# Optimization experiments

Measured on AMD Instinct MI355X. Metric: run time of the kernel, lower is better.

## Reference

```python
import jax, jax.numpy as jnp
import numpy as np

MATCH_TIMES = 4  # init kwarg match_times


def box_xyxy_to_cxcywh(x):
    # x: [..., 4] in (x0, y0, x1, y1)
    x0, y0, x1, y1 = jnp.split(x, 4, axis=-1)
    return jnp.concatenate([(x0 + x1) * 0.5, (y0 + y1) * 0.5, x1 - x0, y1 - y0], axis=-1)


def _pairwise_l1(a, b):
    # a: [B, Q, 4], b: [B, T, 4] -> [B, Q, T] L1 cost matrix
    return jnp.sum(jnp.abs(a[:, :, None, :] - b[:, None, :, :]), axis=-1)


def setup_inputs() -> dict:
    key = jax.random.key(0)
    k1, k2, k3 = jax.random.split(key, 3)
    B, Q, T = 8, 32768, 64
    pred_boxes = jax.random.uniform(k1, (B, Q, 4), dtype=jnp.float32)
    anchors = jax.random.uniform(k2, (B, Q, 4), dtype=jnp.float32)
    gt_boxes = jax.random.uniform(k3, (B, T, 4), dtype=jnp.float32)
    return {"pred_boxes": pred_boxes, "anchors": anchors, "gt_boxes": gt_boxes}


def reference(pred_boxes, anchors, gt_boxes):
    B, Q = pred_boxes.shape[:2]
    T = gt_boxes.shape[1]
    mt = MATCH_TIMES

    gt_c = box_xyxy_to_cxcywh(gt_boxes)
    C = _pairwise_l1(box_xyxy_to_cxcywh(pred_boxes), gt_c)   # [B, Q, T]
    C1 = _pairwise_l1(box_xyxy_to_cxcywh(anchors), gt_c)     # [B, Q, T]

    # per-target k SMALLEST-cost query indices (topk(largest=False))
    _, idx = jax.lax.top_k(-jnp.swapaxes(C, 1, 2), mt)    # [B, T, mt]
    _, idx1 = jax.lax.top_k(-jnp.swapaxes(C1, 1, 2), mt)  # [B, T, mt]

    # per target: concat pred-based and anchor-based matches, then hstack over targets
    idx_i = jnp.concatenate([idx, idx1], axis=-1).reshape(B, T * 2 * mt).astype(jnp.int64)
    # per target j-indices: range(mt) twice (as in source), tiled over targets
    j_row = jnp.tile(jnp.concatenate([jnp.arange(mt), jnp.arange(mt)]), T)  # [T*2*mt]
    idx_j = jnp.broadcast_to(j_row, (B, T * 2 * mt)).astype(jnp.int64)
    return idx_i, idx_j
```

## Files before the change

### kernel.cpp

```cpp
#include <hip/hip_runtime.h>
#include <float.h>

constexpr int Bn = 8, Qn = 32768, Tn = 64, MT = 4;
constexpr int BLOCK = 256;
constexpr int CHUNKS = 64;
constexpr int CHUNK  = Qn / CHUNKS;
constexpr int PARTS  = BLOCK / 64;
constexpr int SUB    = CHUNK / PARTS;

__device__ __forceinline__ void cmpx(float& av, int& ai, float& bv, int& bi) {
    bool sw = (bv < av) || ((bv == av) && (bi < ai));
    float v0 = sw ? bv : av; int i0 = sw ? bi : ai;
    float v1 = sw ? av : bv; int i1 = sw ? ai : bi;
    av = v0; ai = i0; bv = v1; bi = i1;
}

__device__ __forceinline__ void merge4(float a_v[4], int a_i[4],
                                       const float b_v[4], const int b_i[4]) {
    float mv[4]; int mi[4];
#pragma unroll
    for (int k = 0; k < 4; ++k) {
        float bv = b_v[3 - k]; int bi = b_i[3 - k];
        bool ta = (a_v[k] < bv) || ((a_v[k] == bv) && (a_i[k] < bi));
        mv[k] = ta ? a_v[k] : bv;
        mi[k] = ta ? a_i[k] : bi;
    }
    cmpx(mv[0], mi[0], mv[2], mi[2]);
    cmpx(mv[1], mi[1], mv[3], mi[3]);
    cmpx(mv[0], mi[0], mv[1], mi[1]);
    cmpx(mv[2], mi[2], mv[3], mi[3]);
#pragma unroll
    for (int k = 0; k < 4; ++k) { a_v[k] = mv[k]; a_i[k] = mi[k]; }
}

__global__ __launch_bounds__(BLOCK) void matcher_stage1(
        const float* __restrict__ pred, const float* __restrict__ anch,
        const float* __restrict__ gt, float2* __restrict__ partial) {
    const int c     = blockIdx.x;
    const int which = blockIdx.y;
    const int b     = blockIdx.z;
    const int tid   = threadIdx.x;

    __shared__ float4 sbox[CHUNK];
    __shared__ float2 sred[PARTS][64][5];

    const float4* bp = (const float4*)((which ? anch : pred) + (size_t)b * Qn * 4)
                       + (size_t)c * CHUNK;
#pragma unroll
    for (int i = tid; i < CHUNK; i += BLOCK) {
        float4 p = bp[i];
        sbox[i] = make_float4((p.x + p.z) * 0.5f, (p.y + p.w) * 0.5f,
                              p.z - p.x, p.w - p.y);
    }

    const int t    = tid & 63;
    const int part = tid >> 6;
    const float4 g = *(const float4*)(gt + ((size_t)b * Tn + t) * 4);
    const float gcx = (g.x + g.z) * 0.5f;
    const float gcy = (g.y + g.w) * 0.5f;
    const float gw  = g.z - g.x;
    const float gh  = g.w - g.y;

    __syncthreads();

    float v[4]  = {FLT_MAX, FLT_MAX, FLT_MAX, FLT_MAX};
    int   ix[4] = {0x7fffffff, 0x7fffffff, 0x7fffffff, 0x7fffffff};

    const int j0 = part * SUB;
    const int qbase = c * CHUNK + j0;
#pragma unroll 8
    for (int jj = 0; jj < SUB; ++jj) {
        float4 p = sbox[j0 + jj];
        float d0 = p.x - gcx, d1 = p.y - gcy, d2 = p.z - gw, d3 = p.w - gh;
        float cst = fabsf(d0) + fabsf(d1);
        cst += fabsf(d2);
        cst += fabsf(d3);
        const int q = qbase + jj;
        float n0 = fminf(v[0], cst);
        float n1 = __builtin_amdgcn_fmed3f(v[0], v[1], cst);
        float n2 = __builtin_amdgcn_fmed3f(v[1], v[2], cst);
        float n3 = __builtin_amdgcn_fmed3f(v[2], v[3], cst);
        bool b0 = cst < v[0], b1 = cst < v[1], b2 = cst < v[2], b3 = cst < v[3];
        int i3 = b2 ? ix[2] : (b3 ? q : ix[3]);
        int i2 = b1 ? ix[1] : (b2 ? q : ix[2]);
        int i1 = b0 ? ix[0] : (b1 ? q : ix[1]);
        int i0 = b0 ? q : ix[0];
        v[0] = n0; v[1] = n1; v[2] = n2; v[3] = n3;
        ix[0] = i0; ix[1] = i1; ix[2] = i2; ix[3] = i3;
    }

#pragma unroll
    for (int k = 0; k < 4; ++k)
        sred[part][t][k] = make_float2(v[k], __int_as_float(ix[k]));
    __syncthreads();

    if (tid < 64) {
#pragma unroll
        for (int p2 = 1; p2 < PARTS; ++p2) {
            float bv[4]; int bi[4];
#pragma unroll
            for (int k = 0; k < 4; ++k) {
                float2 e = sred[p2][t][k];
                bv[k] = e.x; bi[k] = __float_as_int(e.y);
            }
            merge4(v, ix, bv, bi);
        }
        const int bw = b * 2 + which;
        float2* dst = partial + (((size_t)bw * CHUNKS + c) * 64 + t) * 4;
#pragma unroll
        for (int k = 0; k < 4; ++k)
            dst[k] = make_float2(v[k], __int_as_float(ix[k]));
    }
}

__global__ __launch_bounds__(BLOCK) void matcher_stage2(
        const float2* __restrict__ partial,
        int* __restrict__ out_i, int* __restrict__ out_j) {
    const int lane = threadIdx.x & 63;
    const int gwv  = blockIdx.x * (BLOCK / 64) + (threadIdx.x >> 6);
    const int bw = gwv >> 6;
    const int t  = gwv & 63;

    const float4* src4 = (const float4*)(partial + (((size_t)bw * CHUNKS + lane) * 64 + t) * 4);
    float4 e0 = src4[0], e1 = src4[1];
    float v[4]; int ix[4];
    v[0] = e0.x; ix[0] = __float_as_int(e0.y);
    v[1] = e0.z; ix[1] = __float_as_int(e0.w);
    v[2] = e1.x; ix[2] = __float_as_int(e1.y);
    v[3] = e1.z; ix[3] = __float_as_int(e1.w);

#pragma unroll
    for (int d = 1; d < 64; d <<= 1) {
        float bv[4]; int bi[4];
#pragma unroll
        for (int k = 0; k < 4; ++k) {
            bv[k] = __shfl_xor(v[k], d, 64);
            bi[k] = __shfl_xor(ix[k], d, 64);
        }
        merge4(v, ix, bv, bi);
    }
    if (lane == 0) {
        const int b = bw >> 1, which = bw & 1;
        const int base = ((b * Tn + t) * 2 + which) * MT;
#pragma unroll
        for (int k = 0; k < 4; ++k) {
            out_i[base + k] = ix[k];
            out_j[base + k] = k;
        }
    }
}

extern "C" void kernel_launch(void* const* d_in, const int* in_sizes, int n_in,
                              void* d_out, int out_size, void* d_ws, size_t ws_size,
                              hipStream_t stream) {
    const float* pred = (const float*)d_in[0];
    const float* anch = (const float*)d_in[1];
    const float* gt   = (const float*)d_in[2];
    int* out = (int*)d_out;
    float2* partial = (float2*)d_ws;
    const int half = Bn * Tn * 2 * MT;

    dim3 grid1(CHUNKS, 2, Bn);
    matcher_stage1<<<grid1, BLOCK, 0, stream>>>(pred, anch, gt, partial);

    const int tuples = Bn * 2 * Tn;
    dim3 grid2(tuples / (BLOCK / 64));
    matcher_stage2<<<grid2, BLOCK, 0, stream>>>(partial, out, out + half);
}
```

Baseline: 83.02 us.

## Fuse two-stage top-k into one kernel with atomic last-blocks reduction

Merges the chunk-level top-k kernel and the final reduction kernel into one launch. Each block bumps a per-(batch,source) atomic counter after writing its partial results. The last FIN blocks to arrive spin until all chunks are done, then each reduces a quarter of the targets. This removes a kernel launch and the gap between launches, but adds a memset, a spin-wait on global memory, and a dependence on all blocks of a group being resident or finished.

```diff
diff --git a/kernel.cpp b/kernel.cpp
--- a/kernel.cpp
+++ b/kernel.cpp
@@ -7,6 +7,8 @@
 constexpr int CHUNK  = Qn / CHUNKS;
 constexpr int PARTS  = BLOCK / 64;
 constexpr int SUB    = CHUNK / PARTS;
+constexpr int NBW    = Bn * 2;
+constexpr int FIN    = 4;
 
 __device__ __forceinline__ void cmpx(float& av, int& ai, float& bv, int& bi) {
     bool sw = (bv < av) || ((bv == av) && (bi < ai));
@@ -33,16 +35,19 @@
     for (int k = 0; k < 4; ++k) { a_v[k] = mv[k]; a_i[k] = mi[k]; }
 }
 
-__global__ __launch_bounds__(BLOCK) void matcher_stage1(
+__global__ __launch_bounds__(BLOCK) void matcher_fused(
         const float* __restrict__ pred, const float* __restrict__ anch,
-        const float* __restrict__ gt, float2* __restrict__ partial) {
+        const float* __restrict__ gt, float2* __restrict__ partial,
+        int* __restrict__ cnt, int* __restrict__ out_i, int* __restrict__ out_j) {
     const int c     = blockIdx.x;
     const int which = blockIdx.y;
     const int b     = blockIdx.z;
     const int tid   = threadIdx.x;
+    const int bw    = b * 2 + which;
 
     __shared__ float4 sbox[CHUNK];
     __shared__ float2 sred[PARTS][64][5];
+    __shared__ int s_old;
 
     const float4* bp = (const float4*)((which ? anch : pred) + (size_t)b * Qn * 4)
                        + (size_t)c * CHUNK;
@@ -105,47 +110,57 @@
             }
             merge4(v, ix, bv, bi);
         }
-        const int bw = b * 2 + which;
         float2* dst = partial + (((size_t)bw * CHUNKS + c) * 64 + t) * 4;
 #pragma unroll
         for (int k = 0; k < 4; ++k)
             dst[k] = make_float2(v[k], __int_as_float(ix[k]));
     }
-}
 
-__global__ __launch_bounds__(BLOCK) void matcher_stage2(
-        const float2* __restrict__ partial,
-        int* __restrict__ out_i, int* __restrict__ out_j) {
-    const int lane = threadIdx.x & 63;
-    const int gwv  = blockIdx.x * (BLOCK / 64) + (threadIdx.x >> 6);
-    const int bw = gwv >> 6;
-    const int t  = gwv & 63;
+    __threadfence();
+    if (tid == 0) s_old = atomicAdd(&cnt[bw], 1);
+    __syncthreads();
+    const int old = s_old;
+    if (old < CHUNKS - FIN) return;
 
-    const float4* src4 = (const float4*)(partial + (((size_t)bw * CHUNKS + lane) * 64 + t) * 4);
-    float4 e0 = src4[0], e1 = src4[1];
-    float v[4]; int ix[4];
-    v[0] = e0.x; ix[0] = __float_as_int(e0.y);
-    v[1] = e0.z; ix[1] = __float_as_int(e0.w);
-    v[2] = e1.x; ix[2] = __float_as_int(e1.y);
-    v[3] = e1.z; ix[3] = __float_as_int(e1.w);
+    if (tid == 0) {
+        while (__hip_atomic_load(&cnt[bw], __ATOMIC_RELAXED,
+                                 __HIP_MEMORY_SCOPE_AGENT) < CHUNKS)
+            __builtin_amdgcn_s_sleep(2);
+    }
+    __syncthreads();
+    __threadfence();
 
+    const int fidx = old - (CHUNKS - FIN);
+    const int lane = tid & 63;
+    const int wv   = tid >> 6;
 #pragma unroll
-    for (int d = 1; d < 64; d <<= 1) {
-        float bv[4]; int bi[4];
+    for (int i = 0; i < 4; ++i) {
+        const int tt = fidx * 16 + wv * 4 + i;
+        const float4* src4 = (const float4*)(partial +
+                (((size_t)bw * CHUNKS + lane) * 64 + tt) * 4);
+        float4 e0 = src4[0], e1 = src4[1];
+        float mv[4]; int mi[4];
+        mv[0] = e0.x; mi[0] = __float_as_int(e0.y);
+        mv[1] = e0.z; mi[1] = __float_as_int(e0.w);
+        mv[2] = e1.x; mi[2] = __float_as_int(e1.y);
+        mv[3] = e1.z; mi[3] = __float_as_int(e1.w);
 #pragma unroll
-        for (int k = 0; k < 4; ++k) {
-            bv[k] = __shfl_xor(v[k], d, 64);
-            bi[k] = __shfl_xor(ix[k], d, 64);
+        for (int d = 1; d < 64; d <<= 1) {
+            float bv[4]; int bi[4];
+#pragma unroll
+            for (int k = 0; k < 4; ++k) {
+                bv[k] = __shfl_xor(mv[k], d, 64);
+                bi[k] = __shfl_xor(mi[k], d, 64);
+            }
+            merge4(mv, mi, bv, bi);
         }
-        merge4(v, ix, bv, bi);
-    }
-    if (lane == 0) {
-        const int b = bw >> 1, which = bw & 1;
-        const int base = ((b * Tn + t) * 2 + which) * MT;
+        if (lane == 0) {
+            const int base = ((b * Tn + tt) * 2 + which) * MT;
 #pragma unroll
-        for (int k = 0; k < 4; ++k) {
-            out_i[base + k] = ix[k];
-            out_j[base + k] = k;
+            for (int k = 0; k < 4; ++k) {
+                out_i[base + k] = mi[k];
+                out_j[base + k] = k;
+            }
         }
     }
 }
@@ -158,12 +173,12 @@
     const float* gt   = (const float*)d_in[2];
     int* out = (int*)d_out;
     float2* partial = (float2*)d_ws;
+    int* cnt = (int*)((char*)d_ws + (size_t)2 * 1024 * 1024);
     const int half = Bn * Tn * 2 * MT;
 
-    dim3 grid1(CHUNKS, 2, Bn);
-    matcher_stage1<<<grid1, BLOCK, 0, stream>>>(pred, anch, gt, partial);
+    hipMemsetAsync(cnt, 0, NBW * sizeof(int), stream);
 
-    const int tuples = Bn * 2 * Tn;
-    dim3 grid2(tuples / (BLOCK / 64));
-    matcher_stage2<<<grid2, BLOCK, 0, stream>>>(partial, out, out + half);
+    dim3 grid(CHUNKS, 2, Bn);
+    matcher_fused<<<grid, BLOCK, 0, stream>>>(pred, anch, gt, partial, cnt,
+                                              out, out + half);
 }
```

Measured after the change: 179.4 us. 2.16x slower.
